# Performance work log

Hardware: AMD Instinct MI355X
Metric: run time of the kernel (lower is better)

Reference implementation:

```python
import jax, jax.numpy as jnp
import numpy as np

B, T, D, H, F = 2, 2048, 1024, 16, 4096
DH = D // H  # 64
EPS = 1e-5


def setup_inputs() -> dict:
    key = jax.random.key(0)
    ks = jax.random.split(key, 12)
    s = 0.02
    return {
        "embedding": jax.random.normal(ks[0], (B, T, D), dtype=jnp.float32),
        "Wq": jax.random.normal(ks[1], (H, D, DH), dtype=jnp.float32) * s,
        "Wk": jax.random.normal(ks[2], (H, D, DH), dtype=jnp.float32) * s,
        "Wv": jax.random.normal(ks[3], (H, D, DH), dtype=jnp.float32) * s,
        "Wo": jax.random.normal(ks[4], (D, D), dtype=jnp.float32) * s,
        "bo": jnp.zeros((D,), dtype=jnp.float32),
        "W1": jax.random.normal(ks[5], (D, F), dtype=jnp.float32) * s,
        "b1": jnp.zeros((F,), dtype=jnp.float32),
        "W2": jax.random.normal(ks[6], (F, D), dtype=jnp.float32) * s,
        "b2": jnp.zeros((D,), dtype=jnp.float32),
        "g1": jnp.ones((D,), dtype=jnp.float32),
        "be1": jnp.zeros((D,), dtype=jnp.float32),
        "g2": jnp.ones((D,), dtype=jnp.float32),
        "be2": jnp.zeros((D,), dtype=jnp.float32),
    }


def _layernorm(x, g, b):
    mu = jnp.mean(x, axis=-1, keepdims=True)
    var = jnp.mean(jnp.square(x - mu), axis=-1, keepdims=True)
    return (x - mu) * jax.lax.rsqrt(var + EPS) * g + b


def reference(embedding, Wq, Wk, Wv, Wo, bo, W1, b1, W2, b2, g1, be1, g2, be2):
    x = embedding  # [B, T, D]
    # per-head projections (no bias), stacked: [B, H, T, DH]
    q = jnp.einsum("btd,hde->bhte", x, Wq)
    k = jnp.einsum("btd,hde->bhte", x, Wk)
    v = jnp.einsum("btd,hde->bhte", x, Wv)
    scores = jnp.einsum("bhte,bhse->bhts", q, k)  # [B, H, T, T]
    mask = jnp.tril(jnp.ones((T, T), dtype=bool))
    # Original masks to -inf first, then scales; -inf * scale = -inf, so this
    # equals softmax(scale * scores) on the causal support.
    scale = DH ** (-0.5)
    scores = jnp.where(mask, scores * scale, -jnp.inf)
    attn = jax.nn.softmax(scores, axis=-1)
    o = jnp.einsum("bhts,bhse->bthe", attn, v).reshape(B, T, D)  # head concat
    attn_out = o @ Wo + bo
    a = x + _layernorm(attn_out, g1, be1)  # residual uses original input
    f = jax.nn.relu(a @ W1 + b1) @ W2 + b2
    out = x + _layernorm(f, g2, be2)  # NOTE: residual from x, as in source
    return out
```

## Files before the change

### kernel.cpp

```cpp
#include <hip/hip_runtime.h>
#include <hip/hip_bf16.h>


#define Bq_ 2
#define T_ 2048
#define D_ 1024
#define H_ 16
#define DH_ 64
#define F_ 4096
#define N_ (Bq_ * T_)
#define EPS_ 1e-5f
#define KP 72

typedef __hip_bfloat16 bf16;
typedef unsigned short u16;
typedef __attribute__((ext_vector_type(8))) short bfrag;
typedef __attribute__((ext_vector_type(4))) float f32x4;

__device__ __forceinline__ u16 f2b(float f) {
    bf16 h = __float2bfloat16(f);
    return *(u16*)&h;
}
__device__ __forceinline__ float b2f_bits(u16 u) {
    return __uint_as_float(((unsigned)u) << 16);
}

__device__ __forceinline__ int swz(int row, int col) {
    return (col & ~31) | ((((col >> 3) ^ (row >> 1)) & 3) << 3) | (col & 7);
}

template <int N>
__device__ __forceinline__ void vmwait() {
    asm volatile("s_waitcnt vmcnt(%0)" :: "i"(N) : "memory");
}

#define GLDS16(g, l) __builtin_amdgcn_global_load_lds( \
    (const __attribute__((address_space(1))) unsigned int*)(g), \
    (__attribute__((address_space(3))) unsigned int*)(l), 16, 0, 0)

__device__ __forceinline__ void tc_body(
    float (*Ts)[65], const float* s, int spitch,
    u16* dst, int dpitch, int drow0, int kcol0)
{
    const int t = threadIdx.x;
    #pragma unroll
    for (int i = 0; i < 4; i++) {
        const int idx = t + i * 256;
        const int kk = idx >> 4;
        const int mm = (idx & 15) * 4;
        float4 v = *(const float4*)(s + (size_t)kk * spitch + mm);
        Ts[mm][kk] = v.x; Ts[mm + 1][kk] = v.y;
        Ts[mm + 2][kk] = v.z; Ts[mm + 3][kk] = v.w;
    }
    __syncthreads();
    const int mm = t >> 2;
    const int kk0 = (t & 3) * 16;
    u16 o[16];
    #pragma unroll
    for (int j = 0; j < 16; j++) o[j] = f2b(Ts[mm][kk0 + j]);
    const int dr = drow0 + mm;
    u16* drow = dst + (size_t)dr * dpitch;
    const int c0 = kcol0 + kk0;
    *(uint4*)&drow[swz(dr, c0)]     = *(uint4*)&o[0];
    *(uint4*)&drow[swz(dr, c0 + 8)] = *(uint4*)&o[8];
}

__global__ __launch_bounds__(256) void tcvt(
    const float* __restrict__ src, int spitch, int srow0, int scol0,
    u16* __restrict__ dst, int dpitch, int drow0)
{
    __shared__ float Ts[64][65];
    const int mb = blockIdx.x, kb = blockIdx.y;
    const float* s = src + (size_t)(srow0 + kb * 64) * spitch + scol0 + mb * 64;
    tc_body(Ts, s, spitch, dst, dpitch, drow0 + mb * 64, kb * 64);
}

__global__ __launch_bounds__(256) void tcvt_kv(
    const float* __restrict__ Wk, const float* __restrict__ Wv,
    u16* __restrict__ dst)
{
    __shared__ float Ts[64][65];
    const int kb = blockIdx.y, z = blockIdx.z;
    const int sel = z >> 4, zz = z & 15;
    const float* src = sel ? Wv : Wk;
    const float* s = src + (size_t)zz * 1024 * 64 + (size_t)(kb * 64) * 64;
    tc_body(Ts, s, 64, dst, 1024, sel * 1024 + zz * 64, kb * 64);
}

__global__ __launch_bounds__(256) void tcvt_ffn(
    const float* __restrict__ W1, const float* __restrict__ W2, int c,
    u16* __restrict__ W1T, u16* __restrict__ W2T)
{
    __shared__ float Ts[64][65];
    const int mb = blockIdx.x, kb = blockIdx.y, z = blockIdx.z;
    const float* src = z ? W2 : W1;
    const int spitch = z ? 1024 : 4096;
    const int srow0  = z ? c * 1024 : 0;
    const int scol0  = z ? 0 : c * 1024;
    u16* dst = z ? W2T : W1T;
    const float* s = src + (size_t)(srow0 + kb * 64) * spitch + scol0 + mb * 64;
    tc_body(Ts, s, spitch, dst, 1024, mb * 64, kb * 64);
}

template <int AF32, int SPLIT, int RELU, int ACC, int NT, int CSWZ, int DEEP>
__global__ __launch_bounds__(256) void cgemm(
    const void* __restrict__ A, int lda,
    const u16* __restrict__ BT,
    u16* __restrict__ C0, u16* __restrict__ C1, int ldc,
    int Kdim,
    const float* __restrict__ bias, int bias_off)
{
    static_assert(NT == 2 || NT == 4, "NT");
    static_assert(!AF32 || NT == 4, "AF32 path assumes BN=128");
    static_assert(!(AF32 && DEEP), "DEEP requires glds-only staging");
    constexpr int BN = NT * 32;
    constexpr int NBUF = DEEP ? 4 : 2;
    constexpr int LPT = (NT == 4) ? 4 : 3;
    __shared__ alignas(16) u16 As[NBUF][BN][32];
    __shared__ alignas(16) u16 Bs[NBUF][128][32];

    const int tid = threadIdx.x;
    const int lane = tid & 63;
    const int w = tid >> 6;
    const int lo16 = lane & 15;
    const int quad = lane >> 4;
    const int wi = w >> 1, wj = w & 1;

    const int m0 = blockIdx.x * 128;
    const int n0 = blockIdx.y * BN;

    f32x4 acc[NT][4] = {};

    const int c8 = (lane & 3) * 8;
    const int r4 = lane >> 2;
    const int br0 = w * 32 + r4;
    const int br1 = br0 + 16;
    const int fcol = ((quad ^ ((lo16 >> 1) & 3)) << 3);

    auto stage = [&](int buf, int k0) {
        GLDS16(BT + (size_t)(m0 + br0) * Kdim + k0 + c8,
               &Bs[buf][0][0] + (w * 2 + 0) * 512);
        GLDS16(BT + (size_t)(m0 + br1) * Kdim + k0 + c8,
               &Bs[buf][0][0] + (w * 2 + 1) * 512);
        if constexpr (AF32) {
            const int ar = tid >> 1;
            const int kh = (tid & 1) * 16;
            const float* ap = (const float*)A + (size_t)(n0 + ar) * lda + k0 + kh;
            float4 v0 = ((const float4*)ap)[0];
            float4 v1 = ((const float4*)ap)[1];
            float4 v2 = ((const float4*)ap)[2];
            float4 v3 = ((const float4*)ap)[3];
            uint4 a0, a1;
            a0.x = (unsigned)f2b(v0.x) | ((unsigned)f2b(v0.y) << 16);
            a0.y = (unsigned)f2b(v0.z) | ((unsigned)f2b(v0.w) << 16);
            a0.z = (unsigned)f2b(v1.x) | ((unsigned)f2b(v1.y) << 16);
            a0.w = (unsigned)f2b(v1.z) | ((unsigned)f2b(v1.w) << 16);
            a1.x = (unsigned)f2b(v2.x) | ((unsigned)f2b(v2.y) << 16);
            a1.y = (unsigned)f2b(v2.z) | ((unsigned)f2b(v2.w) << 16);
            a1.z = (unsigned)f2b(v3.x) | ((unsigned)f2b(v3.y) << 16);
            a1.w = (unsigned)f2b(v3.z) | ((unsigned)f2b(v3.w) << 16);
            *(uint4*)&As[buf][ar][swz(ar, kh)] = a0;
            *(uint4*)&As[buf][ar][swz(ar, kh + 8)] = a1;
        } else {
            const u16* Ab = (const u16*)A;
            if constexpr (NT == 4) {
                GLDS16(Ab + (size_t)(n0 + br0) * lda + k0 + c8,
                       &As[buf][0][0] + (w * 2 + 0) * 512);
                GLDS16(Ab + (size_t)(n0 + br1) * lda + k0 + c8,
                       &As[buf][0][0] + (w * 2 + 1) * 512);
            } else {
                const int ar0 = w * 16 + r4;
                GLDS16(Ab + (size_t)(n0 + ar0) * lda + k0 + c8,
                       &As[buf][0][0] + w * 512);
            }
        }
    };

    const int nsteps = Kdim >> 5;

    if constexpr (DEEP) {
        stage(0, 0); stage(1, 32); stage(2, 64);
        for (int t = 0; t < nsteps; ++t) {
            if (t < nsteps - 2)       vmwait<2 * LPT>();
            else if (t == nsteps - 2) vmwait<LPT>();
            else                      vmwait<0>();
            __builtin_amdgcn_s_barrier();
            __builtin_amdgcn_sched_barrier(0);
            const int cb = t & 3;
            bfrag af[NT], bfv[4];
            #pragma unroll
            for (int it = 0; it < NT; it++)
                af[it] = *(const bfrag*)&As[cb][wi * (NT * 16) + it * 16 + lo16][fcol];
            #pragma unroll
            for (int jt = 0; jt < 4; jt++)
                bfv[jt] = *(const bfrag*)&Bs[cb][wj * 64 + jt * 16 + lo16][fcol];
            if (t + 3 < nsteps) stage((t + 3) & 3, (t + 3) * 32);
            __builtin_amdgcn_s_setprio(1);
            #pragma unroll
            for (int it = 0; it < NT; it++)
                #pragma unroll
                for (int jt = 0; jt < 4; jt++)
                    acc[it][jt] = __builtin_amdgcn_mfma_f32_16x16x32_bf16(
                        af[it], bfv[jt], acc[it][jt], 0, 0, 0);
            __builtin_amdgcn_s_setprio(0);
        }
        __builtin_amdgcn_s_barrier();
    } else {
        stage(0, 0);
        __syncthreads();
        int cur = 0;
        for (int t = 0; t < nsteps; ++t) {
            if (t + 1 < nsteps) stage(cur ^ 1, (t + 1) * 32);
            bfrag af[NT], bfv[4];
            #pragma unroll
            for (int it = 0; it < NT; it++)
                af[it] = *(const bfrag*)&As[cur][wi * (NT * 16) + it * 16 + lo16][fcol];
            #pragma unroll
            for (int jt = 0; jt < 4; jt++)
                bfv[jt] = *(const bfrag*)&Bs[cur][wj * 64 + jt * 16 + lo16][fcol];
            __builtin_amdgcn_s_setprio(1);
            #pragma unroll
            for (int it = 0; it < NT; it++)
                #pragma unroll
                for (int jt = 0; jt < 4; jt++)
                    acc[it][jt] = __builtin_amdgcn_mfma_f32_16x16x32_bf16(
                        af[it], bfv[jt], acc[it][jt], 0, 0, 0);
            __builtin_amdgcn_s_setprio(0);
            if (t + 1 < nsteps) {
                __syncthreads();
                cur ^= 1;
            }
        }
    }
    #pragma unroll
    for (int jt = 0; jt < 4; jt++) {
        const int col = m0 + wj * 64 + jt * 16 + lo16;
        u16* Cp;
        int cc;
        if constexpr (SPLIT) {
            Cp = (col >> 10) ? C1 : C0;
            cc = col & 1023;
        } else {
            Cp = C0;
            cc = col;
        }
        const float bv = bias ? bias[bias_off + col] : 0.f;
        #pragma unroll
        for (int it = 0; it < NT; it++) {
            #pragma unroll
            for (int r = 0; r < 4; r++) {
                const int row = n0 + wi * (NT * 16) + it * 16 + quad * 4 + r;
                float v = acc[it][jt][r] + bv;
                if constexpr (RELU) v = fmaxf(v, 0.f);
                const int ccs = CSWZ ? swz(row, cc) : cc;
                u16* cp = Cp + (size_t)row * ldc + ccs;
                if constexpr (ACC) v += b2f_bits(*cp);
                *cp = f2b(v);
            }
        }
    }
}

template <int AF32, int QKV, int RELU, int ACC>
__global__ __launch_bounds__(256) void mgemm(
    const void* __restrict__ A,
    const float* __restrict__ B0f, const float* __restrict__ B1f, const float* __restrict__ B2f,
    u16* __restrict__ C0, u16* __restrict__ C1, u16* __restrict__ C2,
    int ldb, int brow_off, int bcol_off,
    const float* __restrict__ bias, int bias_off)
{
    __shared__ alignas(16) u16 As[128][32];
    __shared__ alignas(16) u16 Bt[128][40];
    __shared__ alignas(16) float Bs32[32][132];

    const int tid = threadIdx.x;
    const int lane = tid & 63;
    const int w = tid >> 6;
    const int lo16 = lane & 15;
    const int quad = lane >> 4;
    const int wi = w >> 1, wj = w & 1;

    const int m0 = blockIdx.x * 128;
    const int n0 = blockIdx.y * 128;

    f32x4 acc[4][4] = {};

    const int ar  = tid >> 1;
    const int akh = (tid & 1) * 16;
    const int bmq = tid & 31;
    const int bkb = (tid >> 5) * 4;
    const int tm  = tid >> 1;
    const int tkh = (tid & 1) * 16;

    for (int k0 = 0; k0 < 1024; k0 += 32) {
        uint4 a0, a1;
        if constexpr (AF32) {
            const float* ap = (const float*)A + (size_t)(n0 + ar) * 1024 + k0 + akh;
            float4 v0 = ((const float4*)ap)[0];
            float4 v1 = ((const float4*)ap)[1];
            float4 v2 = ((const float4*)ap)[2];
            float4 v3 = ((const float4*)ap)[3];
            a0.x = (unsigned)f2b(v0.x) | ((unsigned)f2b(v0.y) << 16);
            a0.y = (unsigned)f2b(v0.z) | ((unsigned)f2b(v0.w) << 16);
            a0.z = (unsigned)f2b(v1.x) | ((unsigned)f2b(v1.y) << 16);
            a0.w = (unsigned)f2b(v1.z) | ((unsigned)f2b(v1.w) << 16);
            a1.x = (unsigned)f2b(v2.x) | ((unsigned)f2b(v2.y) << 16);
            a1.y = (unsigned)f2b(v2.z) | ((unsigned)f2b(v2.w) << 16);
            a1.z = (unsigned)f2b(v3.x) | ((unsigned)f2b(v3.y) << 16);
            a1.w = (unsigned)f2b(v3.z) | ((unsigned)f2b(v3.w) << 16);
        } else {
            const u16* ap = (const u16*)A + (size_t)(n0 + ar) * 1024 + k0 + akh;
            a0 = ((const uint4*)ap)[0];
            a1 = ((const uint4*)ap)[1];
        }
        #pragma unroll
        for (int kk = 0; kk < 4; kk++) {
            const int k = bkb + kk;
            const float* bp;
            if constexpr (QKV) {
                const int m = m0 + bmq * 4;
                const int sel = m >> 10;
                const int mm = m & 1023;
                const float* Wp = (sel == 0) ? B0f : ((sel == 1) ? B1f : B2f);
                bp = Wp + ((size_t)(mm >> 6) * 1024 + k0 + k) * 64 + (mm & 63);
            } else {
                bp = B0f + (size_t)(brow_off + k0 + k) * ldb + bcol_off + m0 + bmq * 4;
            }
            *(float4*)&Bs32[k][bmq * 4] = *(const float4*)bp;
        }
        __syncthreads();
        *(uint4*)&As[ar][akh] = a0;
        *(uint4*)&As[ar][akh + 8] = a1;
        {
            u16 t[16];
            #pragma unroll
            for (int i = 0; i < 16; i++) t[i] = f2b(Bs32[tkh + i][tm]);
            *(uint4*)&Bt[tm][tkh] = *(uint4*)&t[0];
            *(uint4*)&Bt[tm][tkh + 8] = *(uint4*)&t[8];
        }
        __syncthreads();
        bfrag af[4], bfv[4];
        #pragma unroll
        for (int it = 0; it < 4; it++)
            af[it] = *(const bfrag*)&As[wi * 64 + it * 16 + lo16][quad * 8];
        #pragma unroll
        for (int jt = 0; jt < 4; jt++)
            bfv[jt] = *(const bfrag*)&Bt[wj * 64 + jt * 16 + lo16][quad * 8];
        #pragma unroll
        for (int it = 0; it < 4; it++)
            #pragma unroll
            for (int jt = 0; jt < 4; jt++)
                acc[it][jt] = __builtin_amdgcn_mfma_f32_16x16x32_bf16(
                    af[it], bfv[jt], acc[it][jt], 0, 0, 0);
        __syncthreads();
    }
    #pragma unroll
    for (int jt = 0; jt < 4; jt++) {
        const int col = m0 + wj * 64 + jt * 16 + lo16;
        u16* Cp;
        int cc;
        if constexpr (QKV) {
            const int sel = col >> 10;
            cc = col & 1023;
            Cp = (sel == 0) ? C0 : ((sel == 1) ? C1 : C2);
        } else {
            Cp = C0;
            cc = col;
        }
        const float bv = bias ? bias[bias_off + col] : 0.f;
        #pragma unroll
        for (int it = 0; it < 4; it++) {
            #pragma unroll
            for (int r = 0; r < 4; r++) {
                const int row = n0 + wi * 64 + it * 16 + quad * 4 + r;
                float v = acc[it][jt][r] + bv;
                if constexpr (RELU) v = fmaxf(v, 0.f);
                u16* cp = Cp + (size_t)row * 1024 + cc;
                if constexpr (ACC) v += b2f_bits(*cp);
                *cp = f2b(v);
            }
        }
    }
}

__global__ __launch_bounds__(256) void fattn_kernel(
    u16* __restrict__ Q, const u16* __restrict__ Kg, const u16* __restrict__ Vg)
{
    const int bi = blockIdx.x;
    const int qp = bi & 15;
    const int h  = (bi >> 4) & 15;
    const int b  = bi >> 8;
    const int tid = threadIdx.x;
    const int w = tid >> 6;
    const int lane = tid & 63;
    const int lo16 = lane & 15;
    const int quad = lane >> 4;

    __shared__ alignas(16) u16 Ks[64][KP];
    __shared__ alignas(16) u16 Vt[64][KP];
    __shared__ alignas(16) u16 Ps[4][16][KP];

    const int sr = tid >> 2;
    const int ec = (tid & 3) * 16;

    #pragma unroll 1
    for (int pi = 0; pi < 2; pi++) {
        const int qt = pi ? (31 - qp) : qp;
        const int q0 = qt * 64;
        const size_t qrow = (size_t)(b * T_ + q0 + w * 16 + lo16) * 1024 + h * 64;
        bfrag qa0 = *(const bfrag*)(Q + qrow + quad * 8);
        bfrag qa1 = *(const bfrag*)(Q + qrow + 32 + quad * 8);

        f32x4 oacc[4] = {};
        float m_r[4], l_r[4];
        #pragma unroll
        for (int r = 0; r < 4; r++) { m_r[r] = -3e38f; l_r[r] = 0.f; }

        uint4 ka, kb, va, vb;
        {
            const size_t grow = (size_t)(b * T_ + sr) * 1024 + h * 64 + ec;
            ka = *(const uint4*)(Kg + grow);
            kb = *(const uint4*)(Kg + grow + 8);
            va = *(const uint4*)(Vg + grow);
            vb = *(const uint4*)(Vg + grow + 8);
        }

        for (int st = 0; st <= qt; st++) {
            *(uint4*)&Ks[sr][ec] = ka;
            *(uint4*)&Ks[sr][ec + 8] = kb;
            {
                unsigned vv[8] = {va.x, va.y, va.z, va.w, vb.x, vb.y, vb.z, vb.w};
                #pragma unroll
                for (int k2 = 0; k2 < 8; k2++) {
                    Vt[ec + 2 * k2][sr]     = (u16)(vv[k2] & 0xffff);
                    Vt[ec + 2 * k2 + 1][sr] = (u16)(vv[k2] >> 16);
                }
            }
            __syncthreads();
            if (st < qt) {
                const size_t grow = (size_t)(b * T_ + (st + 1) * 64 + sr) * 1024
                                  + h * 64 + ec;
                ka = *(const uint4*)(Kg + grow);
                kb = *(const uint4*)(Kg + grow + 8);
                va = *(const uint4*)(Vg + grow);
                vb = *(const uint4*)(Vg + grow + 8);
            }

            float sv[4][4];
            #pragma unroll
            for (int nt = 0; nt < 4; nt++) {
                bfrag kb0 = *(const bfrag*)&Ks[nt * 16 + lo16][quad * 8];
                bfrag kb1 = *(const bfrag*)&Ks[nt * 16 + lo16][32 + quad * 8];
                f32x4 cs = {0.f, 0.f, 0.f, 0.f};
                cs = __builtin_amdgcn_mfma_f32_16x16x32_bf16(qa0, kb0, cs, 0, 0, 0);
                cs = __builtin_amdgcn_mfma_f32_16x16x32_bf16(qa1, kb1, cs, 0, 0, 0);
                #pragma unroll
                for (int r = 0; r < 4; r++) sv[nt][r] = cs[r] * 0.125f;
            }
            if (st == qt) {
                #pragma unroll
                for (int nt = 0; nt < 4; nt++)
                    #pragma unroll
                    for (int r = 0; r < 4; r++)
                        if (nt * 16 + lo16 > w * 16 + quad * 4 + r) sv[nt][r] = -3e38f;
            }
            #pragma unroll
            for (int r = 0; r < 4; r++) {
                float m = fmaxf(fmaxf(sv[0][r], sv[1][r]), fmaxf(sv[2][r], sv[3][r]));
                #pragma unroll
                for (int off = 1; off < 16; off <<= 1)
                    m = fmaxf(m, __shfl_xor(m, off, 64));
                float mnew = fmaxf(m_r[r], m);
                float alpha = __expf(m_r[r] - mnew);
                m_r[r] = mnew;
                float s = 0.f;
                #pragma unroll
                for (int nt = 0; nt < 4; nt++) {
                    sv[nt][r] = __expf(sv[nt][r] - mnew);
                    s += sv[nt][r];
                }
                #pragma unroll
                for (int off = 1; off < 16; off <<= 1)
                    s += __shfl_xor(s, off, 64);
                l_r[r] = l_r[r] * alpha + s;
                #pragma unroll
                for (int et = 0; et < 4; et++) oacc[et][r] *= alpha;
            }
            #pragma unroll
            for (int nt = 0; nt < 4; nt++)
                #pragma unroll
                for (int r = 0; r < 4; r++)
                    Ps[w][quad * 4 + r][nt * 16 + lo16] = f2b(sv[nt][r]);
            bfrag pa0 = *(const bfrag*)&Ps[w][lo16][quad * 8];
            bfrag pa1 = *(const bfrag*)&Ps[w][lo16][32 + quad * 8];
            #pragma unroll
            for (int et = 0; et < 4; et++) {
                bfrag vb0 = *(const bfrag*)&Vt[et * 16 + lo16][quad * 8];
                bfrag vb1 = *(const bfrag*)&Vt[et * 16 + lo16][32 + quad * 8];
                oacc[et] = __builtin_amdgcn_mfma_f32_16x16x32_bf16(pa0, vb0, oacc[et], 0, 0, 0);
                oacc[et] = __builtin_amdgcn_mfma_f32_16x16x32_bf16(pa1, vb1, oacc[et], 0, 0, 0);
            }
            __syncthreads();
        }
        #pragma unroll
        for (int r = 0; r < 4; r++) {
            float rl = 1.f / l_r[r];
            const int row = q0 + w * 16 + quad * 4 + r;
            u16* orow = Q + (size_t)(b * T_ + row) * 1024;
            #pragma unroll
            for (int et = 0; et < 4; et++)
                orow[swz(row, h * 64 + et * 16 + lo16)] = f2b(oacc[et][r] * rl);
        }
    }
}

template <int WF32, int OSWZ>
__global__ __launch_bounds__(256) void ln_kernel(
    const u16* __restrict__ src, const float* __restrict__ resid,
    const float* __restrict__ g, const float* __restrict__ be,
    u16* __restrict__ dstb, float* __restrict__ dstf)
{
    const int r = blockIdx.x;
    const int tid = threadIdx.x;
    uint2 raw = ((const uint2*)(src + (size_t)r * D_))[tid];
    float y[4];
    y[0] = __uint_as_float(raw.x << 16);
    y[1] = __uint_as_float(raw.x & 0xffff0000u);
    y[2] = __uint_as_float(raw.y << 16);
    y[3] = __uint_as_float(raw.y & 0xffff0000u);
    float s = y[0] + y[1] + y[2] + y[3];
    float sq = y[0]*y[0] + y[1]*y[1] + y[2]*y[2] + y[3]*y[3];
    #pragma unroll
    for (int o = 32; o > 0; o >>= 1) {
        s += __shfl_down(s, o, 64);
        sq += __shfl_down(sq, o, 64);
    }
    __shared__ float rs[4], rq[4];
    if ((tid & 63) == 0) { rs[tid >> 6] = s; rq[tid >> 6] = sq; }
    __syncthreads();
    const float S = rs[0] + rs[1] + rs[2] + rs[3];
    const float Qm = rq[0] + rq[1] + rq[2] + rq[3];
    const float mu = S * (1.f / (float)D_);
    const float var = fmaxf(Qm * (1.f / (float)D_) - mu * mu, 0.f);
    const float rstd = rsqrtf(var + EPS_);
    const int c = tid * 4;
    #pragma unroll
    for (int i = 0; i < 4; i++) {
        y[i] = (y[i] - mu) * rstd * g[c + i] + be[c + i]
             + resid[(size_t)r * D_ + c + i];
    }
    if constexpr (WF32) {
        float4 o = {y[0], y[1], y[2], y[3]};
        ((float4*)(dstf + (size_t)r * D_))[tid] = o;
    } else {
        uint2 o;
        o.x = (unsigned)f2b(y[0]) | ((unsigned)f2b(y[1]) << 16);
        o.y = (unsigned)f2b(y[2]) | ((unsigned)f2b(y[3]) << 16);
        const int cs = OSWZ ? swz(r, c) : c;
        *(uint2*)(dstb + (size_t)r * D_ + cs) = o;
    }
}

extern "C" void kernel_launch(void* const* d_in, const int* in_sizes, int n_in,
                              void* d_out, int out_size, void* d_ws, size_t ws_size,
                              hipStream_t stream)
{
    const float* emb = (const float*)d_in[0];
    const float* Wq  = (const float*)d_in[1];
    const float* Wk  = (const float*)d_in[2];
    const float* Wv  = (const float*)d_in[3];
    const float* Wo  = (const float*)d_in[4];
    const float* bo  = (const float*)d_in[5];
    const float* W1  = (const float*)d_in[6];
    const float* b1  = (const float*)d_in[7];
    const float* W2  = (const float*)d_in[8];
    const float* b2  = (const float*)d_in[9];
    const float* g1  = (const float*)d_in[10];
    const float* be1 = (const float*)d_in[11];
    const float* g2  = (const float*)d_in[12];
    const float* be2 = (const float*)d_in[13];

    u16* WS = (u16*)d_ws;
    u16* DO = (u16*)d_out;

    const size_t M1 = 1024 * 1024;
    u16* WkvT = WS;
    u16* Q    = WS;
    u16* Kb   = DO;
    u16* Vb   = DO + 4 * M1;
    u16* O    = WS;
    u16* WoT  = DO;
    u16* P    = DO + 4 * M1;
    u16* Af   = DO;
    u16* Hc   = DO + 4 * M1;
    u16* W1T  = DO + 6 * M1;
    u16* W2T  = DO + 7 * M1;
    u16* F    = WS;
    float* outf = (float*)d_out;

    const dim3 blk(256);

    tcvt_kv<<<dim3(1, 16, 32), blk, 0, stream>>>(Wk, Wv, WkvT);
    cgemm<1, 1, 0, 0, 4, 0, 0><<<dim3(16, 32), blk, 0, stream>>>(
        emb, 1024, WkvT, Kb, Vb, 1024, 1024, nullptr, 0);
    mgemm<1, 1, 0, 0><<<dim3(8, 32), blk, 0, stream>>>(
        emb, Wq, Wq, Wq, Q, nullptr, nullptr, 0, 0, 0, nullptr, 0);
    fattn_kernel<<<Bq_ * H_ * 16, blk, 0, stream>>>(Q, Kb, Vb);
    tcvt<<<dim3(16, 16), blk, 0, stream>>>(Wo, 1024, 0, 0, WoT, 1024, 0);
    cgemm<0, 0, 0, 0, 4, 0, 1><<<dim3(8, 32), blk, 0, stream>>>(
        O, 1024, WoT, P, nullptr, 1024, 1024, bo, 0);
    ln_kernel<0, 1><<<N_, blk, 0, stream>>>(P, emb, g1, be1, Af, nullptr);
    for (int c = 0; c < 4; c++) {
        tcvt_ffn<<<dim3(16, 16, 2), blk, 0, stream>>>(W1, W2, c, W1T, W2T);
        for (int rh = 0; rh < 2; rh++) {
            u16* Afh = Af + (size_t)rh * 2048 * 1024;
            u16* Fh  = F  + (size_t)rh * 2048 * 1024;
            cgemm<0, 0, 1, 0, 2, 1, 1><<<dim3(8, 32), blk, 0, stream>>>(
                Afh, 1024, W1T, Hc, nullptr, 1024, 1024, b1, c * 1024);
            if (c == 0) {
                cgemm<0, 0, 0, 0, 2, 0, 1><<<dim3(8, 32), blk, 0, stream>>>(
                    Hc, 1024, W2T, Fh, nullptr, 1024, 1024, b2, 0);
            } else {
                cgemm<0, 0, 0, 1, 2, 0, 1><<<dim3(8, 32), blk, 0, stream>>>(
                    Hc, 1024, W2T, Fh, nullptr, 1024, 1024, nullptr, 0);
            }
        }
    }
    ln_kernel<1, 0><<<N_, blk, 0, stream>>>(F, emb, g2, be2, nullptr, outf);
}
```

Baseline: 603.4 us.

## Replace block-shared deep pipeline with per-wave private staging buffers in GEMM

```diff
diff --git a/kernel.cpp b/kernel.cpp
--- a/kernel.cpp
+++ b/kernel.cpp
@@ -102,7 +102,7 @@
     tc_body(Ts, s, spitch, dst, 1024, mb * 64, kb * 64);
 }
 
-template <int AF32, int SPLIT, int RELU, int ACC, int NT, int CSWZ, int DEEP>
+template <int AF32, int SPLIT, int RELU, int ACC, int NT, int CSWZ, int WAVE>
 __global__ __launch_bounds__(256) void cgemm(
     const void* __restrict__ A, int lda,
     const u16* __restrict__ BT,
@@ -112,12 +112,17 @@
 {
     static_assert(NT == 2 || NT == 4, "NT");
     static_assert(!AF32 || NT == 4, "AF32 path assumes BN=128");
-    static_assert(!(AF32 && DEEP), "DEEP requires glds-only staging");
+    static_assert(!(AF32 && WAVE), "WAVE requires glds-only staging");
     constexpr int BN = NT * 32;
-    constexpr int NBUF = DEEP ? 4 : 2;
-    constexpr int LPT = (NT == 4) ? 4 : 3;
-    __shared__ alignas(16) u16 As[NBUF][BN][32];
-    __shared__ alignas(16) u16 Bs[NBUF][128][32];
+    constexpr int NBUF = (NT == 2) ? 5 : 4;
+    constexpr int DPT  = NBUF - 1;
+    constexpr int LPT  = 4 + NT;
+    constexpr int BELEM = 64 * 32;
+    constexpr int AELEM = NT * 16 * 32;
+    constexpr int PBUF  = BELEM + AELEM;
+    constexpr int SELEM = WAVE ? 4 * NBUF * PBUF
+                               : 2 * BN * 32 + 2 * 128 * 32;
+    __shared__ alignas(16) u16 SMEM[SELEM];
 
     const int tid = threadIdx.x;
     const int lane = tid & 63;
@@ -133,16 +138,82 @@
 
     const int c8 = (lane & 3) * 8;
     const int r4 = lane >> 2;
-    const int br0 = w * 32 + r4;
-    const int br1 = br0 + 16;
     const int fcol = ((quad ^ ((lo16 >> 1) & 3)) << 3);
 
-    auto stage = [&](int buf, int k0) {
-        GLDS16(BT + (size_t)(m0 + br0) * Kdim + k0 + c8,
-               &Bs[buf][0][0] + (w * 2 + 0) * 512);
-        GLDS16(BT + (size_t)(m0 + br1) * Kdim + k0 + c8,
-               &Bs[buf][0][0] + (w * 2 + 1) * 512);
-        if constexpr (AF32) {
+    const int nsteps = Kdim >> 5;
+
+    if constexpr (WAVE) {
+        const u16* Ab = (const u16*)A;
+        u16* wbase = &SMEM[w * NBUF * PBUF];
+        auto wstage = [&](int slot, int k0) {
+            u16* bb = wbase + slot * PBUF;
+            #pragma unroll
+            for (int c = 0; c < 4; c++)
+                GLDS16(BT + (size_t)(m0 + wj * 64 + c * 16 + r4) * Kdim + k0 + c8,
+                       bb + c * 512);
+            u16* ab = bb + BELEM;
+            #pragma unroll
+            for (int c = 0; c < NT; c++)
+                GLDS16(Ab + (size_t)(n0 + wi * (NT * 16) + c * 16 + r4) * lda + k0 + c8,
+                       ab + c * 512);
+        };
+        #pragma unroll
+        for (int i = 0; i < DPT; i++) wstage(i, i * 32);
+        int t = 0, cb = 0;
+        for (; t + DPT <= nsteps; ++t) {
+            vmwait<(DPT - 1) * LPT>();
+            __builtin_amdgcn_sched_barrier(0);
+            const u16* bb = wbase + cb * PBUF;
+            const u16* ab = bb + BELEM;
+            bfrag af[NT], bfv[4];
+            #pragma unroll
+            for (int it = 0; it < NT; it++)
+                af[it] = *(const bfrag*)(ab + (it * 16 + lo16) * 32 + fcol);
+            #pragma unroll
+            for (int jt = 0; jt < 4; jt++)
+                bfv[jt] = *(const bfrag*)(bb + (jt * 16 + lo16) * 32 + fcol);
+            if (t + DPT < nsteps)
+                wstage(cb == 0 ? NBUF - 1 : cb - 1, (t + DPT) * 32);
+            __builtin_amdgcn_s_setprio(1);
+            #pragma unroll
+            for (int it = 0; it < NT; it++)
+                #pragma unroll
+                for (int jt = 0; jt < 4; jt++)
+                    acc[it][jt] = __builtin_amdgcn_mfma_f32_16x16x32_bf16(
+                        af[it], bfv[jt], acc[it][jt], 0, 0, 0);
+            __builtin_amdgcn_s_setprio(0);
+            cb = (cb + 1 == NBUF) ? 0 : cb + 1;
+        }
+        vmwait<0>();
+        __builtin_amdgcn_sched_barrier(0);
+        for (; t < nsteps; ++t) {
+            const u16* bb = wbase + cb * PBUF;
+            const u16* ab = bb + BELEM;
+            bfrag af[NT], bfv[4];
+            #pragma unroll
+            for (int it = 0; it < NT; it++)
+                af[it] = *(const bfrag*)(ab + (it * 16 + lo16) * 32 + fcol);
+            #pragma unroll
+            for (int jt = 0; jt < 4; jt++)
+                bfv[jt] = *(const bfrag*)(bb + (jt * 16 + lo16) * 32 + fcol);
+            #pragma unroll
+            for (int it = 0; it < NT; it++)
+                #pragma unroll
+                for (int jt = 0; jt < 4; jt++)
+                    acc[it][jt] = __builtin_amdgcn_mfma_f32_16x16x32_bf16(
+                        af[it], bfv[jt], acc[it][jt], 0, 0, 0);
+            cb = (cb + 1 == NBUF) ? 0 : cb + 1;
+        }
+    } else {
+        u16* As_ = SMEM;
+        u16* Bs_ = SMEM + 2 * BN * 32;
+        const int br0 = w * 32 + r4;
+        const int br1 = br0 + 16;
+        auto stage = [&](int buf, int k0) {
+            GLDS16(BT + (size_t)(m0 + br0) * Kdim + k0 + c8,
+                   Bs_ + buf * 128 * 32 + (w * 2 + 0) * 512);
+            GLDS16(BT + (size_t)(m0 + br1) * Kdim + k0 + c8,
+                   Bs_ + buf * 128 * 32 + (w * 2 + 1) * 512);
             const int ar = tid >> 1;
             const int kh = (tid & 1) * 16;
             const float* ap = (const float*)A + (size_t)(n0 + ar) * lda + k0 + kh;
@@ -159,53 +230,10 @@
             a1.y = (unsigned)f2b(v2.z) | ((unsigned)f2b(v2.w) << 16);
             a1.z = (unsigned)f2b(v3.x) | ((unsigned)f2b(v3.y) << 16);
             a1.w = (unsigned)f2b(v3.z) | ((unsigned)f2b(v3.w) << 16);
-            *(uint4*)&As[buf][ar][swz(ar, kh)] = a0;
-            *(uint4*)&As[buf][ar][swz(ar, kh + 8)] = a1;
-        } else {
-            const u16* Ab = (const u16*)A;
-            if constexpr (NT == 4) {
-                GLDS16(Ab + (size_t)(n0 + br0) * lda + k0 + c8,
-                       &As[buf][0][0] + (w * 2 + 0) * 512);
-                GLDS16(Ab + (size_t)(n0 + br1) * lda + k0 + c8,
-                       &As[buf][0][0] + (w * 2 + 1) * 512);
-            } else {
-                const int ar0 = w * 16 + r4;
-                GLDS16(Ab + (size_t)(n0 + ar0) * lda + k0 + c8,
-                       &As[buf][0][0] + w * 512);
-            }
-        }
-    };
-
-    const int nsteps = Kdim >> 5;
-
-    if constexpr (DEEP) {
-        stage(0, 0); stage(1, 32); stage(2, 64);
-        for (int t = 0; t < nsteps; ++t) {
-            if (t < nsteps - 2)       vmwait<2 * LPT>();
-            else if (t == nsteps - 2) vmwait<LPT>();
-            else                      vmwait<0>();
-            __builtin_amdgcn_s_barrier();
-            __builtin_amdgcn_sched_barrier(0);
-            const int cb = t & 3;
-            bfrag af[NT], bfv[4];
-            #pragma unroll
-            for (int it = 0; it < NT; it++)
-                af[it] = *(const bfrag*)&As[cb][wi * (NT * 16) + it * 16 + lo16][fcol];
-            #pragma unroll
-            for (int jt = 0; jt < 4; jt++)
-                bfv[jt] = *(const bfrag*)&Bs[cb][wj * 64 + jt * 16 + lo16][fcol];
-            if (t + 3 < nsteps) stage((t + 3) & 3, (t + 3) * 32);
-            __builtin_amdgcn_s_setprio(1);
-            #pragma unroll
-            for (int it = 0; it < NT; it++)
-                #pragma unroll
-                for (int jt = 0; jt < 4; jt++)
-                    acc[it][jt] = __builtin_amdgcn_mfma_f32_16x16x32_bf16(
-                        af[it], bfv[jt], acc[it][jt], 0, 0, 0);
-            __builtin_amdgcn_s_setprio(0);
-        }
-        __builtin_amdgcn_s_barrier();
-    } else {
+            u16* arow = As_ + buf * BN * 32 + ar * 32;
+            *(uint4*)&arow[swz(ar, kh)] = a0;
+            *(uint4*)&arow[swz(ar, kh + 8)] = a1;
+        };
         stage(0, 0);
         __syncthreads();
         int cur = 0;
@@ -214,10 +242,12 @@
             bfrag af[NT], bfv[4];
             #pragma unroll
             for (int it = 0; it < NT; it++)
-                af[it] = *(const bfrag*)&As[cur][wi * (NT * 16) + it * 16 + lo16][fcol];
+                af[it] = *(const bfrag*)(As_ + cur * BN * 32
+                         + (wi * (NT * 16) + it * 16 + lo16) * 32 + fcol);
             #pragma unroll
             for (int jt = 0; jt < 4; jt++)
-                bfv[jt] = *(const bfrag*)&Bs[cur][wj * 64 + jt * 16 + lo16][fcol];
+                bfv[jt] = *(const bfrag*)(Bs_ + cur * 128 * 32
+                          + (wj * 64 + jt * 16 + lo16) * 32 + fcol);
             __builtin_amdgcn_s_setprio(1);
             #pragma unroll
             for (int it = 0; it < NT; it++)
@@ -386,7 +416,8 @@
 __global__ __launch_bounds__(256) void fattn_kernel(
     u16* __restrict__ Q, const u16* __restrict__ Kg, const u16* __restrict__ Vg)
 {
-    const int bi = blockIdx.x;
+    const int bo_ = blockIdx.x;
+    const int bi = ((bo_ & 7) << 6) | (bo_ >> 3);
     const int qp = bi & 15;
     const int h  = (bi >> 4) & 15;
     const int b  = bi >> 8;
```

Measured after the change: 558.5 us. 1.08x faster.
